# Kernel tuning notes

Hardware: AMD Instinct MI355X
Metric: run time of the kernel (lower is better)

The kernel has to match this reference:

```python
import jax, jax.numpy as jnp
import numpy as np

N, E, DI, DO = 100000, 1600000, 64, 64
EPS = 1e-6


def setup_inputs() -> dict:
    key = jax.random.key(0)
    k1, k2, k3, k4 = jax.random.split(key, 4)
    x = jax.random.normal(k1, (N, DI), dtype=jnp.float32)
    src = jax.random.randint(k2, (E,), 0, N, dtype=jnp.int64)
    tgt = jax.random.randint(k3, (E,), 0, N, dtype=jnp.int64)
    kf, kw = jax.random.split(k4)
    # Xavier-uniform init, torch Linear layout: W [out, in]
    limf = float(np.sqrt(6.0 / (2 * DI + DO)))
    limw = float(np.sqrt(6.0 / (2 * DI + 1)))
    Wf = jax.random.uniform(kf, (DO, 2 * DI), jnp.float32, -limf, limf)
    bf = jnp.zeros((DO,), jnp.float32)
    Ww = jax.random.uniform(kw, (1, 2 * DI), jnp.float32, -limw, limw)
    bw = jnp.zeros((1,), jnp.float32)
    return {"x": x, "Wf": Wf, "bf": bf, "Ww": Ww, "bw": bw,
            "src": src, "tgt": tgt, "num_nodes": N}


def reference(x, Wf, bf, Ww, bw, src, tgt, num_nodes):
    # gather endpoints and build edge features [E, 2*di]
    h = jnp.concatenate([x[src], x[tgt]], axis=1)
    y = jax.nn.relu(h @ Wf.T + bf)            # [E, do]
    a = h @ Ww.T + bw                          # [E, 1]
    # global (all-edge) max for numerical stability, as in the original
    a_exp = jnp.exp(a - jnp.max(a, axis=0, keepdims=True))
    # Mtgt @ v  ==  segment_sum(v, tgt)
    a_sum = jax.ops.segment_sum(a_exp, tgt, num_segments=num_nodes) + EPS  # [N, 1]
    o = jax.ops.segment_sum(y * a_exp, tgt, num_segments=num_nodes) / a_sum  # [N, do]
    return o
```

## Files before the change

### kernel.cpp

```cpp
#include <hip/hip_runtime.h>
#include <math.h>


#define DID 64
#define DOD 64
#define SCAN_CHUNK 1024
#define TN 128
#define LDA 129
#define LDB 129

__device__ __forceinline__ unsigned f2key(float f) {
  unsigned u = __float_as_uint(f);
  return (u & 0x80000000u) ? ~u : (u | 0x80000000u);
}
__device__ __forceinline__ float key2f(unsigned k) {
  unsigned u = (k & 0x80000000u) ? (k ^ 0x80000000u) : ~k;
  return __uint_as_float(u);
}

__global__ __launch_bounds__(256, 2) void node_uv_kernel(
    const float* __restrict__ x, const float* __restrict__ Wf,
    const float* __restrict__ Ww, int N,
    float* __restrict__ u, float* __restrict__ v,
    float* __restrict__ p, float* __restrict__ q,
    unsigned* __restrict__ pqmax_key) {
  __shared__ float xT[64 * LDA];
  __shared__ float wT[64 * LDB];
  __shared__ float Wsv[128];

  const int tid = threadIdx.x;

  {
    const float4* wf4 = (const float4*)Wf;
    for (int f4 = tid; f4 < 64 * 32; f4 += 256) {
      int j = f4 >> 5, c4 = (f4 & 31) << 2;
      float4 t = wf4[f4];
      float tv[4] = {t.x, t.y, t.z, t.w};
      #pragma unroll
      for (int ci = 0; ci < 4; ++ci) {
        int c = c4 + ci;
        int k  = (c < 64) ? c : (c - 64);
        int jj = (c < 64) ? j : (64 + j);
        wT[k * LDB + jj] = tv[ci];
      }
    }
    if (tid < 128) Wsv[tid] = Ww[tid];
  }

  float pmax = -INFINITY, qmax = -INFINITY;

  const int tn = tid >> 4;
  const int tj = tid & 15;
  const int n0 = tn * 8, j0 = tj * 8;
  const int ntiles = (N + TN - 1) / TN;

  for (int tile = blockIdx.x; tile < ntiles; tile += gridDim.x) {
    const int base = tile * TN;
    __syncthreads();
    {
      const float4* x4 = (const float4*)(x + (size_t)base * DID);
      for (int f4 = tid; f4 < TN * 16; f4 += 256) {
        int n = f4 >> 4, k4 = (f4 & 15) << 2;
        float4 t = (base + n < N) ? x4[f4] : make_float4(0.f, 0.f, 0.f, 0.f);
        xT[(k4 + 0) * LDA + n] = t.x;
        xT[(k4 + 1) * LDA + n] = t.y;
        xT[(k4 + 2) * LDA + n] = t.z;
        xT[(k4 + 3) * LDA + n] = t.w;
      }
    }
    __syncthreads();

    float acc[8][8];
    #pragma unroll
    for (int i = 0; i < 8; ++i)
      #pragma unroll
      for (int jx = 0; jx < 8; ++jx) acc[i][jx] = 0.f;

    #pragma unroll 4
    for (int k = 0; k < 64; ++k) {
      float4 a0 = *(const float4*)&xT[k * LDA + n0];
      float4 a1 = *(const float4*)&xT[k * LDA + n0 + 4];
      float4 b0 = *(const float4*)&wT[k * LDB + j0];
      float4 b1 = *(const float4*)&wT[k * LDB + j0 + 4];
      float av[8] = {a0.x, a0.y, a0.z, a0.w, a1.x, a1.y, a1.z, a1.w};
      float bv[8] = {b0.x, b0.y, b0.z, b0.w, b1.x, b1.y, b1.z, b1.w};
      #pragma unroll
      for (int i = 0; i < 8; ++i)
        #pragma unroll
        for (int jx = 0; jx < 8; ++jx)
          acc[i][jx] = fmaf(av[i], bv[jx], acc[i][jx]);
    }

    #pragma unroll
    for (int i = 0; i < 8; ++i) {
      int n = base + n0 + i;
      if (n < N) {
        float* dst = (j0 < 64) ? (u + (size_t)n * DOD + j0)
                               : (v + (size_t)n * DOD + (j0 - 64));
        *(float4*)dst       = make_float4(acc[i][0], acc[i][1], acc[i][2], acc[i][3]);
        *(float4*)(dst + 4) = make_float4(acc[i][4], acc[i][5], acc[i][6], acc[i][7]);
      }
    }

    if (tid < TN) {
      int n = base + tid;
      if (n < N) {
        float pp = 0.f, qq = 0.f;
        #pragma unroll 8
        for (int k = 0; k < 64; ++k) {
          float xv = xT[k * LDA + tid];
          pp = fmaf(xv, Wsv[k], pp);
          qq = fmaf(xv, Wsv[64 + k], qq);
        }
        p[n] = pp; q[n] = qq;
        pmax = fmaxf(pmax, pp); qmax = fmaxf(qmax, qq);
      }
    }
  }

  #pragma unroll
  for (int o = 32; o >= 1; o >>= 1) {
    pmax = fmaxf(pmax, __shfl_xor(pmax, o));
    qmax = fmaxf(qmax, __shfl_xor(qmax, o));
  }
  if ((tid & 63) == 0) {
    atomicMax(&pqmax_key[0], f2key(pmax));
    atomicMax(&pqmax_key[1], f2key(qmax));
  }
}

__global__ __launch_bounds__(256) void hist_kernel(
    const int* __restrict__ tgt, int E, int* __restrict__ hist) {
  int tid = blockIdx.x * blockDim.x + threadIdx.x;
  int st  = gridDim.x * blockDim.x;
  int e4  = E >> 2;
  const int4* t4p = (const int4*)tgt;
  for (int i = tid; i < e4; i += st) {
    int4 t4 = t4p[i];
    atomicAdd(&hist[t4.x], 1);
    atomicAdd(&hist[t4.y], 1);
    atomicAdd(&hist[t4.z], 1);
    atomicAdd(&hist[t4.w], 1);
  }
  for (int e = (e4 << 2) + tid; e < E; e += st) atomicAdd(&hist[tgt[e]], 1);
}

__global__ __launch_bounds__(256) void scan1_kernel(
    const int* __restrict__ hist, int* __restrict__ rowstart,
    int* __restrict__ bsum, int N) {
  int base = blockIdx.x * SCAN_CHUNK + threadIdx.x * 4;
  int h[4]; int ts = 0;
  #pragma unroll
  for (int j = 0; j < 4; ++j) {
    int i = base + j;
    h[j] = (i < N) ? hist[i] : 0;
    ts += h[j];
  }
  int lane = threadIdx.x & 63, wv = threadIdx.x >> 6;
  int sc = ts;
  #pragma unroll
  for (int o = 1; o < 64; o <<= 1) {
    int t = __shfl_up(sc, o);
    if (lane >= o) sc += t;
  }
  __shared__ int wtot[4];
  if (lane == 63) wtot[wv] = sc;
  __syncthreads();
  int woff = 0;
  for (int w = 0; w < wv; ++w) woff += wtot[w];
  int excl = woff + sc - ts;
  #pragma unroll
  for (int j = 0; j < 4; ++j) {
    int i = base + j;
    if (i < N) rowstart[i] = excl;
    excl += h[j];
  }
  if (threadIdx.x == 0) {
    int tot = 0;
    for (int w = 0; w < 4; ++w) tot += wtot[w];
    bsum[blockIdx.x] = tot;
  }
}

__global__ __launch_bounds__(256) void scan2_kernel(int* __restrict__ bsum, int SB) {
  __shared__ int tmp[256];
  int t = threadIdx.x;
  int s = (t < SB) ? bsum[t] : 0;
  tmp[t] = s;
  __syncthreads();
  int acc = s;
  for (int o = 1; o < 256; o <<= 1) {
    int vv = (t >= o) ? tmp[t - o] : 0;
    __syncthreads();
    acc += vv;
    tmp[t] = acc;
    __syncthreads();
  }
  if (t < SB) bsum[t] = acc - s;
}

__global__ __launch_bounds__(256) void scan3_kernel(
    int* __restrict__ rowstart, int* __restrict__ cursor,
    const int* __restrict__ bsum, int N, int E) {
  int base = blockIdx.x * SCAN_CHUNK + threadIdx.x * 4;
  int off = bsum[blockIdx.x];
  #pragma unroll
  for (int j = 0; j < 4; ++j) {
    int i = base + j;
    if (i < N) {
      int r = rowstart[i] + off;
      rowstart[i] = r;
      cursor[i] = r;
    }
  }
  if (blockIdx.x == 0 && threadIdx.x == 0) rowstart[N] = E;
}

__global__ __launch_bounds__(256) void fill_kernel(
    const int* __restrict__ src, const int* __restrict__ tgt,
    const float* __restrict__ p, const float* __restrict__ q,
    const unsigned* __restrict__ pqmax_key, int E,
    int* __restrict__ cursor, int2* __restrict__ csr,
    unsigned* __restrict__ wmax_key) {
  const float M = key2f(pqmax_key[0]) + key2f(pqmax_key[1]);
  int tid = blockIdx.x * blockDim.x + threadIdx.x;
  int st  = gridDim.x * blockDim.x;
  int e4  = E >> 2;
  const int4* s4p = (const int4*)src;
  const int4* t4p = (const int4*)tgt;
  float wm = 0.f;
  for (int i = tid; i < e4; i += st) {
    int4 s4 = s4p[i], t4 = t4p[i];
    float a0 = p[s4.x] + q[t4.x];
    float a1 = p[s4.y] + q[t4.y];
    float a2 = p[s4.z] + q[t4.z];
    float a3 = p[s4.w] + q[t4.w];
    float w0 = __expf(a0 - M), w1 = __expf(a1 - M);
    float w2 = __expf(a2 - M), w3 = __expf(a3 - M);
    wm = fmaxf(wm, fmaxf(fmaxf(w0, w1), fmaxf(w2, w3)));
    int p0 = atomicAdd(&cursor[t4.x], 1);
    int p1 = atomicAdd(&cursor[t4.y], 1);
    int p2 = atomicAdd(&cursor[t4.z], 1);
    int p3 = atomicAdd(&cursor[t4.w], 1);
    csr[p0] = make_int2(s4.x, __float_as_int(w0));
    csr[p1] = make_int2(s4.y, __float_as_int(w1));
    csr[p2] = make_int2(s4.z, __float_as_int(w2));
    csr[p3] = make_int2(s4.w, __float_as_int(w3));
  }
  for (int e = (e4 << 2) + tid; e < E; e += st) {
    int t = tgt[e], s = src[e];
    float w = __expf(p[s] + q[t] - M);
    wm = fmaxf(wm, w);
    int pos = atomicAdd(&cursor[t], 1);
    csr[pos] = make_int2(s, __float_as_int(w));
  }
  #pragma unroll
  for (int o = 32; o >= 1; o >>= 1) wm = fmaxf(wm, __shfl_xor(wm, o));
  if ((threadIdx.x & 63) == 0) atomicMax(wmax_key, f2key(wm));
}

__global__ __launch_bounds__(256) void gather_kernel(
    const int* __restrict__ rowstart, const int2* __restrict__ csr,
    const float* __restrict__ u, const float* __restrict__ v,
    const float* __restrict__ bf, const unsigned* __restrict__ wmax_key,
    int N, float* __restrict__ o) {
  const int lane = threadIdx.x & 63;
  const float bfl = bf[lane];
  const float epsEff = 1e-6f * key2f(*wmax_key);
  const int wid = blockIdx.x * (blockDim.x >> 6) + (threadIdx.x >> 6);
  const int nw  = gridDim.x * (blockDim.x >> 6);
  for (int n = wid; n < N; n += nw) {
    const int beg = rowstart[n], end = rowstart[n + 1];
    const float vtl = v[(size_t)n * DOD + lane];
    float acc = 0.f, wl = 0.f;
    for (int bb = beg; bb < end; bb += 64) {
      const int idx = bb + lane;
      int2 c = make_int2(0, 0);
      if (idx < end) c = csr[idx];
      float cw = __uint_as_float((unsigned)c.y);
      wl += cw;
      const int cnt4 = (min(64, end - bb) + 3) & ~3;
      for (int j = 0; j < cnt4; j += 4) {
        int s0 = __shfl(c.x, j + 0), s1 = __shfl(c.x, j + 1);
        int s2 = __shfl(c.x, j + 2), s3 = __shfl(c.x, j + 3);
        float w0 = __shfl(cw, j + 0), w1 = __shfl(cw, j + 1);
        float w2 = __shfl(cw, j + 2), w3 = __shfl(cw, j + 3);
        float r0 = u[(size_t)s0 * DOD + lane];
        float r1 = u[(size_t)s1 * DOD + lane];
        float r2 = u[(size_t)s2 * DOD + lane];
        float r3 = u[(size_t)s3 * DOD + lane];
        acc = fmaf(fmaxf(r0 + vtl + bfl, 0.f), w0, acc);
        acc = fmaf(fmaxf(r1 + vtl + bfl, 0.f), w1, acc);
        acc = fmaf(fmaxf(r2 + vtl + bfl, 0.f), w2, acc);
        acc = fmaf(fmaxf(r3 + vtl + bfl, 0.f), w3, acc);
      }
    }
    #pragma unroll
    for (int off = 32; off >= 1; off >>= 1) wl += __shfl_xor(wl, off);
    o[(size_t)n * DOD + lane] = acc / (wl + epsEff);
  }
}

extern "C" void kernel_launch(void* const* d_in, const int* in_sizes, int n_in,
                              void* d_out, int out_size, void* d_ws, size_t ws_size,
                              hipStream_t stream) {
  const float* x  = (const float*)d_in[0];
  const float* Wf = (const float*)d_in[1];
  const float* bf = (const float*)d_in[2];
  const float* Ww = (const float*)d_in[3];
  const int* src = (const int*)d_in[5];
  const int* tgt = (const int*)d_in[6];

  const int N = in_sizes[0] / DID;
  const int E = in_sizes[5];

  int2*  csr = (int2*)d_ws;
  float* u   = (float*)(csr + E);
  float* v   = u + (size_t)N * DOD;
  float* p   = v + (size_t)N * DOD;
  float* q   = p + N;
  int* hist     = (int*)(q + N);
  int* rowstart = hist + N;
  int* cursor   = rowstart + N + 1;
  int* bsum     = cursor + N;
  unsigned* pqmax_key = (unsigned*)(bsum + 256);
  unsigned* wmax_key  = pqmax_key + 2;

  hipMemsetAsync(hist, 0, (size_t)N * sizeof(int), stream);
  hipMemsetAsync(pqmax_key, 0, 3 * sizeof(unsigned), stream);

  const int SB = (N + SCAN_CHUNK - 1) / SCAN_CHUNK;
  const int ntiles = (N + TN - 1) / TN;

  node_uv_kernel<<<ntiles, 256, 0, stream>>>(x, Wf, Ww, N, u, v, p, q, pqmax_key);
  hist_kernel<<<1024, 256, 0, stream>>>(tgt, E, hist);
  scan1_kernel<<<SB, 256, 0, stream>>>(hist, rowstart, bsum, N);
  scan2_kernel<<<1, 256, 0, stream>>>(bsum, SB);
  scan3_kernel<<<SB, 256, 0, stream>>>(rowstart, cursor, bsum, N, E);
  fill_kernel<<<1024, 256, 0, stream>>>(src, tgt, p, q, pqmax_key, E, cursor,
                                        csr, wmax_key);
  gather_kernel<<<2048, 256, 0, stream>>>(rowstart, csr, u, v, bf, wmax_key,
                                          N, (float*)d_out);
}
```

Measured before the change: 435.0 us.

## Fuse histogram into node kernel and recompute edge weights in gather

Merges the target-degree histogram pass into the node projection kernel, which removes one launch. The CSR now holds only source indices (int instead of int2), and each edge's attention weight is recomputed in the gather kernel from p[src] and q[n]. This halves the scattered CSR writes and reads, in exchange for an extra random read of p and an exp per edge in the gather. The fill kernel now tracks the max logit and applies exp only once per wavefront for the epsilon scale.

Result: faster. 387.2 us (-11.0%).

```diff
diff --git a/kernel.cpp b/kernel.cpp
--- a/kernel.cpp
+++ b/kernel.cpp
@@ -23,7 +23,8 @@
     const float* __restrict__ Ww, int N,
     float* __restrict__ u, float* __restrict__ v,
     float* __restrict__ p, float* __restrict__ q,
-    unsigned* __restrict__ pqmax_key) {
+    unsigned* __restrict__ pqmax_key,
+    const int* __restrict__ tgt, int E, int* __restrict__ hist) {
   __shared__ float xT[64 * LDA];
   __shared__ float wT[64 * LDB];
   __shared__ float Wsv[128];
@@ -127,22 +128,21 @@
     atomicMax(&pqmax_key[0], f2key(pmax));
     atomicMax(&pqmax_key[1], f2key(qmax));
   }
-}
-
-__global__ __launch_bounds__(256) void hist_kernel(
-    const int* __restrict__ tgt, int E, int* __restrict__ hist) {
-  int tid = blockIdx.x * blockDim.x + threadIdx.x;
-  int st  = gridDim.x * blockDim.x;
-  int e4  = E >> 2;
-  const int4* t4p = (const int4*)tgt;
-  for (int i = tid; i < e4; i += st) {
-    int4 t4 = t4p[i];
-    atomicAdd(&hist[t4.x], 1);
-    atomicAdd(&hist[t4.y], 1);
-    atomicAdd(&hist[t4.z], 1);
-    atomicAdd(&hist[t4.w], 1);
-  }
-  for (int e = (e4 << 2) + tid; e < E; e += st) atomicAdd(&hist[tgt[e]], 1);
+
+  {
+    int gtid = blockIdx.x * blockDim.x + tid;
+    int gst  = gridDim.x * blockDim.x;
+    int e4   = E >> 2;
+    const int4* t4p = (const int4*)tgt;
+    for (int i = gtid; i < e4; i += gst) {
+      int4 t4 = t4p[i];
+      atomicAdd(&hist[t4.x], 1);
+      atomicAdd(&hist[t4.y], 1);
+      atomicAdd(&hist[t4.z], 1);
+      atomicAdd(&hist[t4.w], 1);
+    }
+    for (int e = (e4 << 2) + gtid; e < E; e += gst) atomicAdd(&hist[tgt[e]], 1);
+  }
 }
 
 __global__ __launch_bounds__(256) void scan1_kernel(
@@ -220,7 +220,7 @@
     const int* __restrict__ src, const int* __restrict__ tgt,
     const float* __restrict__ p, const float* __restrict__ q,
     const unsigned* __restrict__ pqmax_key, int E,
-    int* __restrict__ cursor, int2* __restrict__ csr,
+    int* __restrict__ cursor, int* __restrict__ csr_src,
     unsigned* __restrict__ wmax_key) {
   const float M = key2f(pqmax_key[0]) + key2f(pqmax_key[1]);
   int tid = blockIdx.x * blockDim.x + threadIdx.x;
@@ -235,54 +235,54 @@
     float a1 = p[s4.y] + q[t4.y];
     float a2 = p[s4.z] + q[t4.z];
     float a3 = p[s4.w] + q[t4.w];
-    float w0 = __expf(a0 - M), w1 = __expf(a1 - M);
-    float w2 = __expf(a2 - M), w3 = __expf(a3 - M);
-    wm = fmaxf(wm, fmaxf(fmaxf(w0, w1), fmaxf(w2, w3)));
+    wm = fmaxf(wm, fmaxf(fmaxf(a0, a1), fmaxf(a2, a3)));
     int p0 = atomicAdd(&cursor[t4.x], 1);
     int p1 = atomicAdd(&cursor[t4.y], 1);
     int p2 = atomicAdd(&cursor[t4.z], 1);
     int p3 = atomicAdd(&cursor[t4.w], 1);
-    csr[p0] = make_int2(s4.x, __float_as_int(w0));
-    csr[p1] = make_int2(s4.y, __float_as_int(w1));
-    csr[p2] = make_int2(s4.z, __float_as_int(w2));
-    csr[p3] = make_int2(s4.w, __float_as_int(w3));
+    csr_src[p0] = s4.x;
+    csr_src[p1] = s4.y;
+    csr_src[p2] = s4.z;
+    csr_src[p3] = s4.w;
   }
   for (int e = (e4 << 2) + tid; e < E; e += st) {
     int t = tgt[e], s = src[e];
-    float w = __expf(p[s] + q[t] - M);
-    wm = fmaxf(wm, w);
+    wm = fmaxf(wm, p[s] + q[t]);
     int pos = atomicAdd(&cursor[t], 1);
-    csr[pos] = make_int2(s, __float_as_int(w));
+    csr_src[pos] = s;
   }
   #pragma unroll
   for (int o = 32; o >= 1; o >>= 1) wm = fmaxf(wm, __shfl_xor(wm, o));
-  if ((threadIdx.x & 63) == 0) atomicMax(wmax_key, f2key(wm));
+  if ((threadIdx.x & 63) == 0) atomicMax(wmax_key, f2key(__expf(wm - M)));
 }
 
 __global__ __launch_bounds__(256) void gather_kernel(
-    const int* __restrict__ rowstart, const int2* __restrict__ csr,
+    const int* __restrict__ rowstart, const int* __restrict__ csr_src,
+    const float* __restrict__ p, const float* __restrict__ q,
     const float* __restrict__ u, const float* __restrict__ v,
-    const float* __restrict__ bf, const unsigned* __restrict__ wmax_key,
+    const float* __restrict__ bf, const unsigned* __restrict__ pqmax_key,
+    const unsigned* __restrict__ wmax_key,
     int N, float* __restrict__ o) {
   const int lane = threadIdx.x & 63;
   const float bfl = bf[lane];
+  const float M = key2f(pqmax_key[0]) + key2f(pqmax_key[1]);
   const float epsEff = 1e-6f * key2f(*wmax_key);
   const int wid = blockIdx.x * (blockDim.x >> 6) + (threadIdx.x >> 6);
   const int nw  = gridDim.x * (blockDim.x >> 6);
   for (int n = wid; n < N; n += nw) {
     const int beg = rowstart[n], end = rowstart[n + 1];
     const float vtl = v[(size_t)n * DOD + lane];
+    const float qn  = q[n];
     float acc = 0.f, wl = 0.f;
     for (int bb = beg; bb < end; bb += 64) {
       const int idx = bb + lane;
-      int2 c = make_int2(0, 0);
-      if (idx < end) c = csr[idx];
-      float cw = __uint_as_float((unsigned)c.y);
+      int se = (idx < end) ? csr_src[idx] : 0;
+      float cw = (idx < end) ? __expf(p[se] + qn - M) : 0.f;
       wl += cw;
       const int cnt4 = (min(64, end - bb) + 3) & ~3;
       for (int j = 0; j < cnt4; j += 4) {
-        int s0 = __shfl(c.x, j + 0), s1 = __shfl(c.x, j + 1);
-        int s2 = __shfl(c.x, j + 2), s3 = __shfl(c.x, j + 3);
+        int s0 = __shfl(se, j + 0), s1 = __shfl(se, j + 1);
+        int s2 = __shfl(se, j + 2), s3 = __shfl(se, j + 3);
         float w0 = __shfl(cw, j + 0), w1 = __shfl(cw, j + 1);
         float w2 = __shfl(cw, j + 2), w3 = __shfl(cw, j + 3);
         float r0 = u[(size_t)s0 * DOD + lane];
@@ -314,8 +314,8 @@
   const int N = in_sizes[0] / DID;
   const int E = in_sizes[5];
 
-  int2*  csr = (int2*)d_ws;
-  float* u   = (float*)(csr + E);
+  int*   csr_src = (int*)d_ws;
+  float* u   = (float*)(csr_src + E);
   float* v   = u + (size_t)N * DOD;
   float* p   = v + (size_t)N * DOD;
   float* q   = p + N;
@@ -332,13 +332,13 @@
   const int SB = (N + SCAN_CHUNK - 1) / SCAN_CHUNK;
   const int ntiles = (N + TN - 1) / TN;
 
-  node_uv_kernel<<<ntiles, 256, 0, stream>>>(x, Wf, Ww, N, u, v, p, q, pqmax_key);
-  hist_kernel<<<1024, 256, 0, stream>>>(tgt, E, hist);
+  node_uv_kernel<<<ntiles, 256, 0, stream>>>(x, Wf, Ww, N, u, v, p, q,
+                                             pqmax_key, tgt, E, hist);
   scan1_kernel<<<SB, 256, 0, stream>>>(hist, rowstart, bsum, N);
   scan2_kernel<<<1, 256, 0, stream>>>(bsum, SB);
   scan3_kernel<<<SB, 256, 0, stream>>>(rowstart, cursor, bsum, N, E);
   fill_kernel<<<1024, 256, 0, stream>>>(src, tgt, p, q, pqmax_key, E, cursor,
-                                        csr, wmax_key);
-  gather_kernel<<<2048, 256, 0, stream>>>(rowstart, csr, u, v, bf, wmax_key,
-                                          N, (float*)d_out);
-}
+                                        csr_src, wmax_key);
+  gather_kernel<<<2048, 256, 0, stream>>>(rowstart, csr_src, p, q, u, v, bf,
+                                          pqmax_key, wmax_key, N, (float*)d_out);
+}
```
